# Kernel tuning notes

Hardware: AMD Instinct MI355X
Metric: run time of the kernel (lower is better)

## Reference

```python
import jax, jax.numpy as jnp
import numpy as np

B, L, N, D, H, F = 8, 12, 207, 512, 8, 2048
OUT_LEN, NG, ORDER = 12, 3, 2
EPS = 1e-6


def _ln(x, g, b):
    m = x.mean(-1, keepdims=True)
    v = x.var(-1, keepdims=True)
    return (x - m) / jnp.sqrt(v + 1e-5) * g + b


def _lin_attn(xq, xkv, w, b):
    # STLinearAttention (mask_flag=False): phi(x)=elu(x)+1 linear attention
    q = xq @ w[0] + b[0]
    k = xkv @ w[1] + b[1]
    v = xkv @ w[2] + b[2]
    Bq, Tq, Dm = q.shape
    Tk = k.shape[1]
    E = Dm // H
    q = q.reshape(Bq, Tq, H, E)
    k = k.reshape(Bq, Tk, H, E)
    v = v.reshape(Bq, Tk, H, E)
    qf = jax.nn.elu(q) + 1.0
    kf = jax.nn.elu(k) + 1.0
    kv = jnp.einsum('bshe,bshd->bhed', kf, v)
    z = 1.0 / (jnp.einsum('bthe,bhe->bth', qf, kf.sum(1)) + EPS)
    o = jnp.einsum('bthe,bhed->bthd', qf, kv) * z[..., None]
    return o.reshape(Bq, Tq, Dm) @ w[3] + b[3]


def _forward(x, st, x_mark, adj_mats, enc_qkvo_w, enc_qkvo_b, enc_ffn_w1, enc_ffn_b1,
             enc_ffn_w2, enc_ffn_b2, enc_ln_g, enc_ln_b, dec_self_w, dec_self_b,
             dec_cross_w, dec_cross_b, dec_ffn_w1, dec_ffn_b1, dec_ffn_w2, dec_ffn_b2,
             dec_ln_g, dec_ln_b, tt_w, tt_b, ts_w, ts_b, gcn_w, gcn_b, gcn_bn_g, gcn_bn_b):
    Bq, Lq, Nq, Dm = x.shape
    # ---- temporal encoder layer over flattened (L*N) tokens ----
    xt = x.reshape(Bq, Lq * Nq, Dm)
    h = xt + _lin_attn(xt, xt, enc_qkvo_w, enc_qkvo_b)
    y = _ln(h, enc_ln_g[0], enc_ln_b[0])
    f = jax.nn.gelu(y @ enc_ffn_w1 + enc_ffn_b1) @ enc_ffn_w2 + enc_ffn_b2
    t_out = _ln(y + f, enc_ln_g[1], enc_ln_b[1])
    # ---- spatial decoder layer: self-attn on st, cross-attn to t_out ----
    mem = t_out
    q = st.reshape(Bq, Lq * Nq, Dm)
    q = _ln(q + _lin_attn(q, q, dec_self_w, dec_self_b), dec_ln_g[0], dec_ln_b[0])
    q = _ln(q + _lin_attn(q, mem, dec_cross_w, dec_cross_b), dec_ln_g[1], dec_ln_b[1])
    f = jax.nn.gelu(q @ dec_ffn_w1 + dec_ffn_b1) @ dec_ffn_w2 + dec_ffn_b2
    s_out = _ln(q + f, dec_ln_g[2], dec_ln_b[2]).reshape(Bq, Lq, Nq, Dm)
    t_out = t_out.reshape(Bq, Lq, Nq, Dm)
    # ---- 1x1 conv projections: seq_len->out_len and d_model->nodes ----
    t_out2 = jnp.einsum('ol,blnd->bond', tt_w, t_out) + tt_b[None, :, None, None]  # [B,O,N,D]
    s_out2 = jnp.einsum('md,blnd->blnm', ts_w, s_out) + ts_b                       # [B,L,N,N]
    # ---- per-timestep NGraphConv with static + learned adaptive adjacency ----
    xg = jnp.swapaxes(t_out2, 2, 3)  # [B,O,D,N]
    feats = [xg]
    for s in range(NG):  # static supports, ORDER hops each
        A = adj_mats[:, :, s]
        hcur = xg
        for _ in range(ORDER):
            hcur = jnp.einsum('bodn,nm->bodm', hcur, A)
            feats.append(hcur)
    Aad = s_out2[:, :OUT_LEN]  # learned adaptive adjacency per timestep [B,O,N,N]
    hcur = xg
    for _ in range(ORDER):
        hcur = jnp.einsum('bodn,bonm->bodm', hcur, Aad)
        feats.append(hcur)
    cat = jnp.concatenate(feats, axis=2)  # [B,O,(NG+1)*ORDER*D+D, N] = [B,O,9D,N]
    g = jnp.einsum('odc,bocn->bodn', gcn_w, cat) + gcn_b[None, :, :, None]
    g = g * gcn_bn_g[None, :, :, None] + gcn_bn_b[None, :, :, None]  # BN (eval)
    dts = jnp.swapaxes(g, 2, 3)  # [B,O,N,D]
    return dts, s_out


def setup_inputs() -> dict:
    key = jax.random.key(0)
    ks = iter(jax.random.split(key, 48))
    nrm = lambda shp, s=0.02: jax.random.normal(next(ks), shp, jnp.float32) * s
    CCAT = D * (NG + 1) * ORDER + D  # 4608
    return dict(
        x=jax.random.normal(next(ks), (B, L, N, D), jnp.float32),
        st=jax.random.normal(next(ks), (B, L, N, D), jnp.float32),
        x_mark=jax.random.normal(next(ks), (B, L, 4), jnp.float32),
        adj_mats=jax.random.uniform(next(ks), (N, N, NG), jnp.float32) / N,
        enc_qkvo_w=nrm((4, D, D)), enc_qkvo_b=jnp.zeros((4, D), jnp.float32),
        enc_ffn_w1=nrm((D, F)), enc_ffn_b1=jnp.zeros((F,), jnp.float32),
        enc_ffn_w2=nrm((F, D)), enc_ffn_b2=jnp.zeros((D,), jnp.float32),
        enc_ln_g=jnp.ones((2, D), jnp.float32), enc_ln_b=jnp.zeros((2, D), jnp.float32),
        dec_self_w=nrm((4, D, D)), dec_self_b=jnp.zeros((4, D), jnp.float32),
        dec_cross_w=nrm((4, D, D)), dec_cross_b=jnp.zeros((4, D), jnp.float32),
        dec_ffn_w1=nrm((D, F)), dec_ffn_b1=jnp.zeros((F,), jnp.float32),
        dec_ffn_w2=nrm((F, D)), dec_ffn_b2=jnp.zeros((D,), jnp.float32),
        dec_ln_g=jnp.ones((3, D), jnp.float32), dec_ln_b=jnp.zeros((3, D), jnp.float32),
        tt_w=nrm((OUT_LEN, L), 0.1), tt_b=jnp.zeros((OUT_LEN,), jnp.float32),
        ts_w=nrm((N, D), 0.05), ts_b=jnp.zeros((N,), jnp.float32),
        gcn_w=nrm((OUT_LEN, D, CCAT)), gcn_b=jnp.zeros((OUT_LEN, D), jnp.float32),
        gcn_bn_g=jnp.ones((OUT_LEN, D), jnp.float32), gcn_bn_b=jnp.zeros((OUT_LEN, D), jnp.float32),
    )


def reference(x, st, x_mark, adj_mats, enc_qkvo_w, enc_qkvo_b, enc_ffn_w1, enc_ffn_b1,
              enc_ffn_w2, enc_ffn_b2, enc_ln_g, enc_ln_b, dec_self_w, dec_self_b,
              dec_cross_w, dec_cross_b, dec_ffn_w1, dec_ffn_b1, dec_ffn_w2, dec_ffn_b2,
              dec_ln_g, dec_ln_b, tt_w, tt_b, ts_w, ts_b, gcn_w, gcn_b, gcn_bn_g, gcn_bn_b):
    return _forward(x, st, x_mark, adj_mats, enc_qkvo_w, enc_qkvo_b, enc_ffn_w1, enc_ffn_b1,
                    enc_ffn_w2, enc_ffn_b2, enc_ln_g, enc_ln_b, dec_self_w, dec_self_b,
                    dec_cross_w, dec_cross_b, dec_ffn_w1, dec_ffn_b1, dec_ffn_w2, dec_ffn_b2,
                    dec_ln_g, dec_ln_b, tt_w, tt_b, ts_w, ts_b, gcn_w, gcn_b, gcn_bn_g, gcn_bn_b)
```

## Files before the change

kernel.cpp:

```cpp
#include <hip/hip_runtime.h>
#include <hip/hip_bf16.h>
#include <cstddef>

using bf16 = __hip_bfloat16;
typedef short s8v __attribute__((ext_vector_type(8)));
typedef __bf16 b8v __attribute__((ext_vector_type(8)));
typedef float f4v __attribute__((ext_vector_type(4)));

constexpr int cB = 8, cL = 12, cN = 207, cD = 512, cH = 8, cF = 2048;
constexpr int cO = 12, cNG = 3;
constexpr int cT  = cL * cN;
constexpr int cBT = cB * cT;
constexpr int cE  = cD / cH;
constexpr size_t SZ = (size_t)cBT * cD;
constexpr long DD = (long)cD * cD;

__device__ __forceinline__ float tofl(bf16 v) { return __bfloat162float(v); }
__device__ __forceinline__ bf16 f2b(float v) { return __float2bfloat16(v); }
__device__ __forceinline__ float ldin(const void* p, size_t i, int bf) {
    return bf ? __bfloat162float(((const bf16*)p)[i]) : ((const float*)p)[i];
}
__device__ __forceinline__ void stout(void* p, size_t i, float v, int bf) {
    if (bf) ((bf16*)p)[i] = f2b(v);
    else    ((float*)p)[i] = v;
}
__device__ __forceinline__ float gelu_f(float x) {
    float x3 = x * x * x;
    return 0.5f * x * (1.f + tanhf(0.7978845608028654f * (x + 0.044715f * x3)));
}
__device__ __forceinline__ void gload16(void* lds, const void* g) {
    __builtin_amdgcn_global_load_lds(
        (const __attribute__((address_space(1))) unsigned int*)g,
        (__attribute__((address_space(3))) unsigned int*)lds,
        16, 0, 0);
}

__global__ void detect_kernel(const void* __restrict__ x, int* __restrict__ flag) {
    __shared__ float red[4];
    int t = threadIdx.x;
    float m = 0.f;
    for (int i = t; i < 1024; i += 256) {
        float v = __bfloat162float(((const bf16*)x)[i]);
        if (v != v) v = 1e30f;
        m = fmaxf(m, fabsf(v));
    }
#pragma unroll
    for (int off = 32; off; off >>= 1) m = fmaxf(m, __shfl_down(m, off));
    if ((t & 63) == 0) red[t >> 6] = m;
    __syncthreads();
    if (t == 0) {
        float mm = fmaxf(fmaxf(red[0], red[1]), fmaxf(red[2], red[3]));
        flag[0] = (mm < 1e3f) ? 1 : 0;
    }
}

__global__ void cvt_copy(bf16* __restrict__ dst, const void* __restrict__ src,
                         const int* __restrict__ fl, size_t n, size_t soff) {
    int bf = *fl;
#pragma unroll
    for (int j = 0; j < 4; ++j) {
        size_t i = (size_t)blockIdx.x * 1024 + (size_t)j * 256 + threadIdx.x;
        if (i < n) dst[i] = f2b(ldin(src, soff + i, bf));
    }
}
__global__ void cvt_tr(bf16* __restrict__ dst, const void* __restrict__ src,
                       const int* __restrict__ fl, int K, int N, size_t soff) {
    int bf = *fl;
    size_t idx = (size_t)blockIdx.x * 256 + threadIdx.x;
    if (idx >= (size_t)K * N) return;
    int n = (int)(idx / K), k = (int)(idx % K);
    dst[idx] = f2b(ldin(src, soff + (size_t)k * N + n, bf));
}

__device__ __forceinline__ void xcd_swz(unsigned& bx, unsigned& by, unsigned& bz) {
    unsigned gx = gridDim.x, gy = gridDim.y;
    unsigned nwg = gx * gy * gridDim.z;
    unsigned orig = (blockIdx.z * gy + blockIdx.y) * gx + blockIdx.x;
    unsigned q = nwg >> 3, r = nwg & 7;
    unsigned xcd = orig & 7, sub = orig >> 3;
    unsigned wg = (xcd < r ? xcd * (q + 1) : r * (q + 1) + (xcd - r) * q) + sub;
    bx = wg % gx;
    unsigned t1 = wg / gx;
    by = t1 % gy;
    bz = t1 / gy;
}

template <int BIAS, int ACT, int OUT>
__global__ __launch_bounds__(256) void mgemm_f(
    const bf16* __restrict__ Ab, const bf16* __restrict__ Bb, void* __restrict__ Cb,
    const bf16* __restrict__ bias,
    int M, int N, int K, int lda, int ldb, int ldc,
    long sA, long sB, long sC, int modA, int modB, long aoff0, long boff0)
{
    unsigned bxu, byu, bzu;
    xcd_swz(bxu, byu, bzu);
    int bz = (int)bzu;
    const bf16* A = Ab + aoff0 + (size_t)(modA ? (bz % modA) : bz) * sA;
    const bf16* B = Bb + boff0 + (size_t)(modB ? (bz % modB) : bz) * sB;
    size_t coff = (size_t)bz * sC;

    int m0 = (int)byu * 128, n0 = (int)bxu * 128;
    int tid = threadIdx.x;
    int lane = tid & 63, w = tid >> 6;
    int wm = (w & 1) * 64, wn = (w >> 1) * 64;
    int l16 = lane & 15, quad = lane >> 4;

    __shared__ short As[128 * 32];
    __shared__ short Bs[128 * 32];

    int srow = tid >> 2, scol = (tid & 3) << 3;
    int ar0 = m0 + srow;      if (ar0 >= M) ar0 = M - 1;
    int ar1 = m0 + srow + 64; if (ar1 >= M) ar1 = M - 1;
    int br0 = n0 + srow;      if (br0 >= N) br0 = N - 1;
    int br1 = n0 + srow + 64; if (br1 >= N) br1 = N - 1;
    const bf16* ap0 = A + (size_t)ar0 * lda + scol;
    const bf16* ap1 = A + (size_t)ar1 * lda + scol;
    const bf16* bp0 = B + (size_t)br0 * ldb + scol;
    const bf16* bp1 = B + (size_t)br1 * ldb + scol;
    short* al0 = &As[w * 512];
    short* al1 = &As[2048 + w * 512];
    short* bl0 = &Bs[w * 512];
    short* bl1 = &Bs[2048 + w * 512];

    f4v acc[4][4] = {};

    int nk = K >> 5;
    for (int kk = 0; kk < nk; ++kk) {
        gload16(al0, ap0);
        gload16(al1, ap1);
        gload16(bl0, bp0);
        gload16(bl1, bp1);
        ap0 += 32; ap1 += 32; bp0 += 32; bp1 += 32;
        __syncthreads();
        b8v af[4], bfr[4];
#pragma unroll
        for (int mi = 0; mi < 4; ++mi)
            af[mi] = *(const b8v*)&As[(wm + mi * 16 + l16) * 32 + quad * 8];
#pragma unroll
        for (int ni = 0; ni < 4; ++ni)
            bfr[ni] = *(const b8v*)&Bs[(wn + ni * 16 + l16) * 32 + quad * 8];
#pragma unroll
        for (int mi = 0; mi < 4; ++mi)
#pragma unroll
            for (int ni = 0; ni < 4; ++ni)
                acc[mi][ni] = __builtin_amdgcn_mfma_f32_16x16x32_bf16(af[mi], bfr[ni], acc[mi][ni], 0, 0, 0);
        __syncthreads();
    }

    bf16* Co = (bf16*)Cb;
    float* Cf = (float*)Cb;
#pragma unroll
    for (int mi = 0; mi < 4; ++mi) {
#pragma unroll
        for (int ni = 0; ni < 4; ++ni) {
            int gn = n0 + wn + ni * 16 + l16;
            float bv = 0.f;
            if (BIAS == 1 && gn < N) bv = tofl(bias[gn]);
#pragma unroll
            for (int r = 0; r < 4; ++r) {
                int gm = m0 + wm + mi * 16 + quad * 4 + r;
                if (gm < M && gn < N) {
                    float v = acc[mi][ni][r] + bv;
                    if (BIAS == 2) v += tofl(bias[gm]);
                    if (ACT == 1) v = gelu_f(v);
                    if (ACT == 2) v = v > 0.f ? v + 1.f : expf(v);
                    size_t ci = coff + (size_t)gm * ldc + gn;
                    if (OUT == 0) Co[ci] = f2b(v);
                    else if (OUT == 1) Cf[ci] = v;
                    else Cf[ci] += v;
                }
            }
        }
    }
}

template <bool TRB, int BIAS, int ACT, int OUT>
__global__ __launch_bounds__(256) void mgemm(
    const bf16* __restrict__ Ab, const bf16* __restrict__ Bb, void* __restrict__ Cb,
    const bf16* __restrict__ bias,
    int M, int N, int K, int lda, int ldb, int ldc,
    long sA, long sB, long sC, int modA, int modB, long aoff0, long boff0)
{
    unsigned bxu, byu, bzu;
    xcd_swz(bxu, byu, bzu);
    int bz = (int)bzu;
    const bf16* A = Ab + aoff0 + (size_t)(modA ? (bz % modA) : bz) * sA;
    const bf16* B = Bb + boff0 + (size_t)(modB ? (bz % modB) : bz) * sB;
    size_t coff = (size_t)bz * sC;

    int m0 = (int)byu * 128, n0 = (int)bxu * 128;
    int tid = threadIdx.x;
    int lane = tid & 63, w = tid >> 6;
    int wm = (w & 1) * 64, wn = (w >> 1) * 64;
    int l16 = lane & 15, quad = lane >> 4;

    __shared__ short Asl[128 * 40];
    __shared__ short Bsl[128 * 40];

    f4v acc[4][4] = {};

    for (int k0 = 0; k0 < K; k0 += 32) {
        for (int g = tid; g < 512; g += 256) {
            int r = g >> 2, kg = (g & 3) << 3;
            int gr = m0 + r, gk = k0 + kg;
            s8v val = {0, 0, 0, 0, 0, 0, 0, 0};
            if (gr < M) {
                const short* src = (const short*)A + (size_t)gr * lda + gk;
                if (gk + 8 <= K) val = *(const s8v*)src;
                else {
#pragma unroll
                    for (int j = 0; j < 8; ++j) if (gk + j < K) val[j] = src[j];
                }
            }
            *(s8v*)&Asl[r * 40 + kg] = val;
        }
        if (TRB) {
            for (int g = tid; g < 512; g += 256) {
                int r = g >> 2, kg = (g & 3) << 3;
                int gr = n0 + r, gk = k0 + kg;
                s8v val = {0, 0, 0, 0, 0, 0, 0, 0};
                if (gr < N) {
                    const short* src = (const short*)B + (size_t)gr * ldb + gk;
                    if (gk + 8 <= K) val = *(const s8v*)src;
                    else {
#pragma unroll
                        for (int j = 0; j < 8; ++j) if (gk + j < K) val[j] = src[j];
                    }
                }
                *(s8v*)&Bsl[r * 40 + kg] = val;
            }
        } else {
            for (int g = tid; g < 512; g += 256) {
                int kr = g >> 4, ng = (g & 15) << 3;
                int gk = k0 + kr, gn = n0 + ng;
                s8v val = {0, 0, 0, 0, 0, 0, 0, 0};
                if (gk < K) {
                    const short* src = (const short*)B + (size_t)gk * ldb + gn;
                    if (gn + 8 <= N) val = *(const s8v*)src;
                    else {
#pragma unroll
                        for (int j = 0; j < 8; ++j) if (gn + j < N) val[j] = src[j];
                    }
                }
#pragma unroll
                for (int j = 0; j < 8; ++j) Bsl[(ng + j) * 40 + kr] = val[j];
            }
        }
        __syncthreads();
        b8v af[4], bfr[4];
#pragma unroll
        for (int mi = 0; mi < 4; ++mi)
            af[mi] = *(const b8v*)&Asl[(wm + mi * 16 + l16) * 40 + quad * 8];
#pragma unroll
        for (int ni = 0; ni < 4; ++ni)
            bfr[ni] = *(const b8v*)&Bsl[(wn + ni * 16 + l16) * 40 + quad * 8];
#pragma unroll
        for (int mi = 0; mi < 4; ++mi)
#pragma unroll
            for (int ni = 0; ni < 4; ++ni)
                acc[mi][ni] = __builtin_amdgcn_mfma_f32_16x16x32_bf16(af[mi], bfr[ni], acc[mi][ni], 0, 0, 0);
        __syncthreads();
    }

    bf16* Co = (bf16*)Cb;
    float* Cf = (float*)Cb;
#pragma unroll
    for (int mi = 0; mi < 4; ++mi) {
#pragma unroll
        for (int ni = 0; ni < 4; ++ni) {
            int gn = n0 + wn + ni * 16 + l16;
            float bv = 0.f;
            if (BIAS == 1 && gn < N) bv = tofl(bias[gn]);
#pragma unroll
            for (int r = 0; r < 4; ++r) {
                int gm = m0 + wm + mi * 16 + quad * 4 + r;
                if (gm < M && gn < N) {
                    float v = acc[mi][ni][r] + bv;
                    if (BIAS == 2) v += tofl(bias[gm]);
                    if (ACT == 1) v = gelu_f(v);
                    if (ACT == 2) v = v > 0.f ? v + 1.f : expf(v);
                    size_t ci = coff + (size_t)gm * ldc + gn;
                    if (OUT == 0) Co[ci] = f2b(v);
                    else if (OUT == 1) Cf[ci] = v;
                    else Cf[ci] += v;
                }
            }
        }
    }
}

__global__ __launch_bounds__(256) void kv_part(
    const bf16* __restrict__ Kf, const bf16* __restrict__ V,
    float* __restrict__ kvp, float* __restrict__ ksp)
{
    int bh = blockIdx.x, c = blockIdx.y;
    int b = bh / cH, h = bh % cH;
    int tbase = c * 621, tend = tbase + 621;
    __shared__ float ks[32][64];
    __shared__ float vs[32][64];
    int tid = threadIdx.x;
    int e = tid >> 2, dg = tid & 3;
    float acc[16] = {};
    float ksacc = 0.f;
    for (int t0 = tbase; t0 < tend; t0 += 32) {
        for (int i = tid; i < 32 * 64; i += 256) {
            int tt = i >> 6, ee = i & 63;
            int t = t0 + tt;
            float kk = 0.f, vv = 0.f;
            if (t < tend) {
                size_t off = ((size_t)(b * cT + t)) * cD + h * cE;
                kk = tofl(Kf[off + ee]);
                vv = tofl(V[off + ee]);
            }
            ks[tt][ee] = kk;
            vs[tt][ee] = vv;
        }
        __syncthreads();
        for (int tt = 0; tt < 32; ++tt) {
            float kf = ks[tt][e];
            if (dg == 0) ksacc += kf;
#pragma unroll
            for (int j = 0; j < 16; ++j) acc[j] += kf * vs[tt][dg * 16 + j];
        }
        __syncthreads();
    }
    size_t base = (((size_t)c * 64 + bh) * cE + e) * cE;
#pragma unroll
    for (int j = 0; j < 16; ++j) kvp[base + dg * 16 + j] = acc[j];
    if (dg == 0) ksp[(size_t)c * 4096 + bh * cE + e] = ksacc;
}

__global__ void kv_reduce(const float* __restrict__ kvp, const float* __restrict__ ksp,
                          float* __restrict__ kvf, float* __restrict__ ksf)
{
    size_t idx = (size_t)blockIdx.x * 256 + threadIdx.x;
    if (idx < 262144) {
        float s = kvp[idx] + kvp[262144 + idx] + kvp[2 * 262144 + idx] + kvp[3 * 262144 + idx];
        kvf[idx] = s;
    } else if (idx < 262144 + 4096) {
        size_t i = idx - 262144;
        ksf[i] = ksp[i] + ksp[4096 + i] + ksp[2 * 4096 + i] + ksp[3 * 4096 + i];
    }
}

__global__ __launch_bounds__(64) void attn_o(
    const bf16* __restrict__ Qf, const float* __restrict__ kv,
    const float* __restrict__ ksum, bf16* __restrict__ O)
{
    int g = blockIdx.x;
    int h = g % cH;
    int bt = g / cH;
    int b = bt / cT;
    int bh = b * cH + h;
    int d = threadIdx.x;
    size_t qoff = (size_t)bt * cD + h * cE;
    __shared__ float qs[64];
    float qv = tofl(Qf[qoff + d]);
    qs[d] = qv;
    float p = qv * ksum[bh * cE + d];
#pragma unroll
    for (int s = 32; s; s >>= 1) p += __shfl_down(p, s);
    float denom = __shfl(p, 0);
    __syncthreads();
    float z = 1.f / (denom + 1e-6f);
    const float* kvp = kv + (size_t)bh * cE * cE;
    float acc = 0.f;
#pragma unroll 8
    for (int e = 0; e < 64; ++e) acc += qs[e] * kvp[e * 64 + d];
    O[qoff + d] = f2b(acc * z);
}

template <int DUAL>
__global__ __launch_bounds__(256) void add_ln(
    const bf16* __restrict__ a, const bf16* __restrict__ b,
    const bf16* __restrict__ g, const bf16* __restrict__ be,
    bf16* __restrict__ out, void* __restrict__ dyn_out,
    const int* __restrict__ fl, size_t dyn_off)
{
    int row = blockIdx.x;
    size_t base = (size_t)row * cD;
    int t = threadIdx.x;
    float x0 = tofl(a[base + t]) + tofl(b[base + t]);
    float x1 = tofl(a[base + t + 256]) + tofl(b[base + t + 256]);
    float s1 = x0 + x1, s2 = x0 * x0 + x1 * x1;
#pragma unroll
    for (int off = 32; off; off >>= 1) { s1 += __shfl_down(s1, off); s2 += __shfl_down(s2, off); }
    __shared__ float r1[4], r2[4];
    int w = t >> 6;
    if ((t & 63) == 0) { r1[w] = s1; r2[w] = s2; }
    __syncthreads();
    float S1 = r1[0] + r1[1] + r1[2] + r1[3];
    float S2 = r2[0] + r2[1] + r2[2] + r2[3];
    float mean = S1 * (1.f / cD);
    float var = S2 * (1.f / cD) - mean * mean;
    float inv = rsqrtf(var + 1e-5f);
    float y0 = (x0 - mean) * inv * tofl(g[t]) + tofl(be[t]);
    float y1 = (x1 - mean) * inv * tofl(g[t + 256]) + tofl(be[t + 256]);
    out[base + t] = f2b(y0);
    out[base + t + 256] = f2b(y1);
    if (DUAL) {
        int bf = *fl;
        stout(dyn_out, dyn_off + base + t, y0, bf);
        stout(dyn_out, dyn_off + base + t + 256, y1, bf);
    }
}

__global__ void tout2_kernel(const bf16* __restrict__ tout, const bf16* __restrict__ ttw,
                             const bf16* __restrict__ ttb, bf16* __restrict__ XT)
{
    size_t idx = (size_t)blockIdx.x * 256 + threadIdx.x;
    if (idx >= SZ) return;
    int d = idx & (cD - 1);
    size_t r = idx >> 9;
    int n = (int)(r % cN);
    size_t r2 = r / cN;
    int o = (int)(r2 % cO);
    int b = (int)(r2 / cO);
    float acc = tofl(ttb[o]);
    size_t base = ((size_t)b * cT + n) * cD + d;
#pragma unroll
    for (int l = 0; l < cL; ++l)
        acc += tofl(ttw[o * cL + l]) * tofl(tout[base + (size_t)l * cN * cD]);
    XT[idx] = f2b(acc);
}

__global__ void extract_adjT(const void* __restrict__ adj, bf16* __restrict__ At3,
                             const int* __restrict__ fl)
{
    int bf = *fl;
    int idx = blockIdx.x * 256 + threadIdx.x;
    if (idx >= cNG * cN * cN) return;
    int s = idx / (cN * cN);
    int rem = idx - s * cN * cN;
    int m = rem / cN;
    int n = rem - m * cN;
    At3[((size_t)s * cN + m) * 208 + n] = f2b(ldin(adj, (size_t)(n * cN + m) * cNG + s, bf));
}

__global__ void dts_kernel(const float* __restrict__ g, const bf16* __restrict__ gb,
                           const bf16* __restrict__ bng, const bf16* __restrict__ bnb,
                           void* __restrict__ out, const int* __restrict__ fl)
{
    int bf = *fl;
    size_t idx = (size_t)blockIdx.x * 256 + threadIdx.x;
    if (idx >= SZ) return;
    int d = idx & (cD - 1);
    size_t r = idx >> 9;
    int o = (int)((r / cN) % cO);
    int od = o * cD + d;
    float v = (g[idx] + tofl(gb[od])) * tofl(bng[od]) + tofl(bnb[od]);
    stout(out, idx, v, bf);
}

static inline dim3 g2(int M, int N, int bz) { return dim3((N + 127) / 128, (M + 127) / 128, bz); }

static void run_attn(const bf16* Aq, const bf16* Akv, const bf16* wT, const bf16* bias,
                     bf16* Q, bf16* K, bf16* V, bf16* outp,
                     float* kvp, float* ksp, float* kvf, float* ksf, hipStream_t s)
{
    mgemm_f<1, 2, 0><<<g2(cBT, cD, 1), 256, 0, s>>>(Aq,  wT,          Q, bias,          cBT, cD, cD, cD, cD, cD, 0, 0, 0, 1, 1, 0, 0);
    mgemm_f<1, 2, 0><<<g2(cBT, cD, 1), 256, 0, s>>>(Akv, wT + DD,     K, bias + cD,     cBT, cD, cD, cD, cD, cD, 0, 0, 0, 1, 1, 0, 0);
    mgemm_f<1, 0, 0><<<g2(cBT, cD, 1), 256, 0, s>>>(Akv, wT + 2 * DD, V, bias + 2 * cD, cBT, cD, cD, cD, cD, cD, 0, 0, 0, 1, 1, 0, 0);
    kv_part<<<dim3(64, 4), 256, 0, s>>>(K, V, kvp, ksp);
    kv_reduce<<<1041, 256, 0, s>>>(kvp, ksp, kvf, ksf);
    attn_o<<<cBT * cH, 64, 0, s>>>(Q, kvf, ksf, Q);
    mgemm_f<1, 0, 0><<<g2(cBT, cD, 1), 256, 0, s>>>(Q, wT + 3 * DD, outp, bias + 3 * cD, cBT, cD, cD, cD, cD, cD, 0, 0, 0, 1, 1, 0, 0);
}

static void run_ffn(const bf16* inp, const bf16* w1T, const bf16* b1,
                    const bf16* w2T, const bf16* b2, bf16* mid, bf16* outp, hipStream_t s)
{
    const int MH = cBT / 2;
    for (int h = 0; h < 2; ++h) {
        const bf16* ip = inp + (size_t)h * MH * cD;
        bf16* op = outp + (size_t)h * MH * cD;
        mgemm_f<1, 1, 0><<<g2(MH, cF, 1), 256, 0, s>>>(ip, w1T, mid, b1, MH, cF, cD, cD, cD, cF, 0, 0, 0, 1, 1, 0, 0);
        mgemm_f<1, 0, 0><<<g2(MH, cD, 1), 256, 0, s>>>(mid, w2T, op, b2, MH, cD, cF, cF, cF, cD, 0, 0, 0, 1, 1, 0, 0);
    }
}

extern "C" void kernel_launch(void* const* d_in, const int* in_sizes, int n_in,
                              void* d_out, int out_size, void* d_ws, size_t ws_size,
                              hipStream_t stream)
{
    const void* x    = d_in[0];
    const void* st   = d_in[1];
    const void* adj  = d_in[3];
    const void* eqw  = d_in[4];
    const void* eqb  = d_in[5];
    const void* ew1  = d_in[6];
    const void* eb1  = d_in[7];
    const void* ew2  = d_in[8];
    const void* eb2  = d_in[9];
    const void* elng = d_in[10];
    const void* elnb = d_in[11];
    const void* dsw  = d_in[12];
    const void* dsb  = d_in[13];
    const void* dcw  = d_in[14];
    const void* dcb  = d_in[15];
    const void* dw1  = d_in[16];
    const void* db1  = d_in[17];
    const void* dw2  = d_in[18];
    const void* db2  = d_in[19];
    const void* dlng = d_in[20];
    const void* dlnb = d_in[21];
    const void* ttw  = d_in[22];
    const void* ttb  = d_in[23];
    const void* tsw  = d_in[24];
    const void* tsb  = d_in[25];
    const void* gw   = d_in[26];
    const void* gb   = d_in[27];
    const void* bng  = d_in[28];
    const void* bnb  = d_in[29];

    bf16* P = (bf16*)d_ws;
    size_t off = 0;
    auto alloc = [&](size_t n) { size_t o = off; off += (n + 127) & ~(size_t)127; return o; };

    size_t eqwT = alloc(4 * DD);
    size_t dswT = alloc(4 * DD);
    size_t dcwT = alloc(4 * DD);
    size_t ew1T = alloc((size_t)cD * cF);
    size_t ew2T = alloc((size_t)cD * cF);
    size_t dw1T = alloc((size_t)cD * cF);
    size_t dw2T = alloc((size_t)cD * cF);
    size_t gwB  = alloc((size_t)cO * cD * 4608);
    size_t tswB = alloc((size_t)cN * cD);
    size_t xb   = alloc(SZ);
    size_t stb  = alloc(SZ);
    size_t eqbB = alloc(4 * cD), eb1B = alloc(cF), eb2B = alloc(cD);
    size_t elngB = alloc(2 * cD), elnbB = alloc(2 * cD);
    size_t dsbB = alloc(4 * cD), dcbB = alloc(4 * cD);
    size_t db1B = alloc(cF), db2B = alloc(cD);
    size_t dlngB = alloc(3 * cD), dlnbB = alloc(3 * cD);
    size_t ttwB = alloc(cO * cL), ttbB = alloc(cO), tsbB = alloc(cN);
    size_t gbB = alloc(cO * cD), bngB = alloc(cO * cD), bnbB = alloc(cO * cD);
    size_t at3 = alloc((size_t)cNG * cN * 208);
    size_t slots = alloc(6 * SZ);
    bf16* S[6];
    for (int i = 0; i < 6; ++i) S[i] = P + slots + (size_t)i * SZ;

    float* F0  = (float*)(P + off);
    float* kvp = F0;
    float* ksp = kvp + 1048576;
    float* kvf = ksp + 16384;
    float* ksf = kvf + 262144;
    int* flag  = (int*)(ksf + 4096);

    detect_kernel<<<1, 256, 0, stream>>>(x, flag);

    for (int i = 0; i < 4; ++i) {
        cvt_tr<<<1024, 256, 0, stream>>>(P + eqwT + i * DD, eqw, flag, cD, cD, (size_t)i * DD);
        cvt_tr<<<1024, 256, 0, stream>>>(P + dswT + i * DD, dsw, flag, cD, cD, (size_t)i * DD);
        cvt_tr<<<1024, 256, 0, stream>>>(P + dcwT + i * DD, dcw, flag, cD, cD, (size_t)i * DD);
    }
    cvt_tr<<<4096, 256, 0, stream>>>(P + ew1T, ew1, flag, cD, cF, 0);
    cvt_tr<<<4096, 256, 0, stream>>>(P + ew2T, ew2, flag, cF, cD, 0);
    cvt_tr<<<4096, 256, 0, stream>>>(P + dw1T, dw1, flag, cD, cF, 0);
    cvt_tr<<<4096, 256, 0, stream>>>(P + dw2T, dw2, flag, cF, cD, 0);
    cvt_copy<<<27648, 256, 0, stream>>>(P + gwB, gw, flag, (size_t)cO * cD * 4608, 0);
    cvt_copy<<<104, 256, 0, stream>>>(P + tswB, tsw, flag, (size_t)cN * cD, 0);
    cvt_copy<<<(int)((SZ + 1023) / 1024), 256, 0, stream>>>(P + xb, x, flag, SZ, 0);
    cvt_copy<<<(int)((SZ + 1023) / 1024), 256, 0, stream>>>(P + stb, st, flag, SZ, 0);
    cvt_copy<<<2, 256, 0, stream>>>(P + eqbB, eqb, flag, 4 * cD, 0);
    cvt_copy<<<2, 256, 0, stream>>>(P + eb1B, eb1, flag, cF, 0);
    cvt_copy<<<1, 256, 0, stream>>>(P + eb2B, eb2, flag, cD, 0);
    cvt_copy<<<1, 256, 0, stream>>>(P + elngB, elng, flag, 2 * cD, 0);
    cvt_copy<<<1, 256, 0, stream>>>(P + elnbB, elnb, flag, 2 * cD, 0);
    cvt_copy<<<2, 256, 0, stream>>>(P + dsbB, dsb, flag, 4 * cD, 0);
    cvt_copy<<<2, 256, 0, stream>>>(P + dcbB, dcb, flag, 4 * cD, 0);
    cvt_copy<<<2, 256, 0, stream>>>(P + db1B, db1, flag, cF, 0);
    cvt_copy<<<1, 256, 0, stream>>>(P + db2B, db2, flag, cD, 0);
    cvt_copy<<<2, 256, 0, stream>>>(P + dlngB, dlng, flag, 3 * cD, 0);
    cvt_copy<<<2, 256, 0, stream>>>(P + dlnbB, dlnb, flag, 3 * cD, 0);
    cvt_copy<<<1, 256, 0, stream>>>(P + ttwB, ttw, flag, cO * cL, 0);
    cvt_copy<<<1, 256, 0, stream>>>(P + ttbB, ttb, flag, cO, 0);
    cvt_copy<<<1, 256, 0, stream>>>(P + tsbB, tsb, flag, cN, 0);
    cvt_copy<<<6, 256, 0, stream>>>(P + gbB, gb, flag, cO * cD, 0);
    cvt_copy<<<6, 256, 0, stream>>>(P + bngB, bng, flag, cO * cD, 0);
    cvt_copy<<<6, 256, 0, stream>>>(P + bnbB, bnb, flag, cO * cD, 0);

    run_attn(P + xb, P + xb, P + eqwT, P + eqbB, S[0], S[1], S[2], S[3], kvp, ksp, kvf, ksf, stream);
    add_ln<0><<<cBT, 256, 0, stream>>>(P + xb, S[3], P + elngB, P + elnbB, S[4], nullptr, flag, 0);
    run_ffn(S[4], P + ew1T, P + eb1B, P + ew2T, P + eb2B, S[0], S[2], stream);
    add_ln<0><<<cBT, 256, 0, stream>>>(S[4], S[2], P + elngB + cD, P + elnbB + cD, S[5], nullptr, flag, 0);

    run_attn(P + stb, P + stb, P + dswT, P + dsbB, S[0], S[1], S[2], S[3], kvp, ksp, kvf, ksf, stream);
    add_ln<0><<<cBT, 256, 0, stream>>>(P + stb, S[3], P + dlngB, P + dlnbB, S[4], nullptr, flag, 0);

    run_attn(S[4], S[5], P + dcwT, P + dcbB, S[0], S[1], S[2], S[3], kvp, ksp, kvf, ksf, stream);
    add_ln<0><<<cBT, 256, 0, stream>>>(S[4], S[3], P + dlngB + cD, P + dlnbB + cD, S[4], nullptr, flag, 0);

    run_ffn(S[4], P + dw1T, P + db1B, P + dw2T, P + db2B, S[0], S[2], stream);
    add_ln<1><<<cBT, 256, 0, stream>>>(S[4], S[2], P + dlngB + 2 * cD, P + dlnbB + 2 * cD, S[3], d_out, flag, SZ);

    tout2_kernel<<<(int)(SZ / 256), 256, 0, stream>>>(S[5], P + ttwB, P + ttbB, S[0]);

    mgemm_f<2, 0, 0><<<g2(cN, cN, cB * cO), 256, 0, stream>>>(
        P + tswB, S[3], S[1], P + tsbB, cN, cN, cD, cD, cD, 208,
        0, (long)cN * cD, (long)cN * 208, 1, 0, 0, 0);

    extract_adjT<<<(cNG * cN * cN + 255) / 256, 256, 0, stream>>>(adj, P + at3, flag);

    float* G = (float*)S[4];

    auto accum = [&](const bf16* Feat, int f) {
        mgemm_f<0, 0, 2><<<g2(cN, cD, cB * cO), 256, 0, stream>>>(
            Feat, P + gwB, G, nullptr, cN, cD, cD, cD, 4608, cD,
            (long)cN * cD, (long)cD * 4608, (long)cN * cD, 0, cO, 0, (long)f * cD);
    };
    auto featmul = [&](const bf16* A, long sA, int modA, long aoff0, const bf16* Fin, bf16* Fout) {
        mgemm<false, 0, 0, 0><<<g2(cN, cD, cB * cO), 256, 0, stream>>>(
            A, Fin, Fout, nullptr, cN, cD, cN, 208, cD, cD,
            sA, (long)cN * cD, (long)cN * cD, modA, 0, aoff0, 0);
    };

    mgemm_f<0, 0, 1><<<g2(cN, cD, cB * cO), 256, 0, stream>>>(
        S[0], P + gwB, G, nullptr, cN, cD, cD, cD, 4608, cD,
        (long)cN * cD, (long)cD * 4608, (long)cN * cD, 0, cO, 0, 0);
    for (int s = 0; s < cNG; ++s) {
        featmul(P + at3, 0, 1, (long)s * cN * 208, S[0], S[3]);
        accum(S[3], 2 * s + 1);
        featmul(P + at3, 0, 1, (long)s * cN * 208, S[3], S[2]);
        accum(S[2], 2 * s + 2);
    }
    featmul(S[1], (long)cN * 208, 0, 0, S[0], S[3]);
    accum(S[3], 7);
    featmul(S[1], (long)cN * 208, 0, 0, S[3], S[2]);
    accum(S[2], 8);

    dts_kernel<<<(int)((SZ + 255) / 256), 256, 0, stream>>>(G, P + gbB, P + bngB, P + bnbB, d_out, flag);
}
```

Baseline: 2.586 ms.

## Split KV accumulation into 12 chunks, tile attention output per chunk, vectorize tout2

```diff
diff --git a/kernel.cpp b/kernel.cpp
--- a/kernel.cpp
+++ b/kernel.cpp
@@ -14,9 +14,19 @@
 constexpr int cE  = cD / cH;
 constexpr size_t SZ = (size_t)cBT * cD;
 constexpr long DD = (long)cD * cD;
+constexpr int KVCH = 12;
+constexpr int CHLEN = 207;
 
 __device__ __forceinline__ float tofl(bf16 v) { return __bfloat162float(v); }
 __device__ __forceinline__ bf16 f2b(float v) { return __float2bfloat16(v); }
+__device__ __forceinline__ float b2f_raw(short s) {
+    unsigned u = ((unsigned)(unsigned short)s) << 16;
+    float f; __builtin_memcpy(&f, &u, 4); return f;
+}
+__device__ __forceinline__ short f2b_raw(float v) {
+    bf16 t = __float2bfloat16(v);
+    short s; __builtin_memcpy(&s, &t, 2); return s;
+}
 __device__ __forceinline__ float ldin(const void* p, size_t i, int bf) {
     return bf ? __bfloat162float(((const bf16*)p)[i]) : ((const float*)p)[i];
 }
@@ -294,39 +304,51 @@
     float* __restrict__ kvp, float* __restrict__ ksp)
 {
     int bh = blockIdx.x, c = blockIdx.y;
-    int b = bh / cH, h = bh % cH;
-    int tbase = c * 621, tend = tbase + 621;
+    int b = bh >> 3, h = bh & 7;
+    int tbase = c * CHLEN, tend = tbase + CHLEN;
     __shared__ float ks[32][64];
     __shared__ float vs[32][64];
     int tid = threadIdx.x;
     int e = tid >> 2, dg = tid & 3;
-    float acc[16] = {};
+    f4v a0 = {}, a1 = {}, a2 = {}, a3 = {};
     float ksacc = 0.f;
+    int srow = tid >> 3, sc = (tid & 7) << 3;
     for (int t0 = tbase; t0 < tend; t0 += 32) {
-        for (int i = tid; i < 32 * 64; i += 256) {
-            int tt = i >> 6, ee = i & 63;
-            int t = t0 + tt;
-            float kk = 0.f, vv = 0.f;
-            if (t < tend) {
-                size_t off = ((size_t)(b * cT + t)) * cD + h * cE;
-                kk = tofl(Kf[off + ee]);
-                vv = tofl(V[off + ee]);
-            }
-            ks[tt][ee] = kk;
-            vs[tt][ee] = vv;
+        int t = t0 + srow;
+        s8v kk8 = {0, 0, 0, 0, 0, 0, 0, 0};
+        s8v vv8 = {0, 0, 0, 0, 0, 0, 0, 0};
+        if (t < tend) {
+            size_t off2 = ((size_t)(b * cT + t)) * cD + h * cE + sc;
+            kk8 = *(const s8v*)((const short*)Kf + off2);
+            vv8 = *(const s8v*)((const short*)V + off2);
         }
         __syncthreads();
+        f4v kf0, kf1, vf0, vf1;
+#pragma unroll
+        for (int j = 0; j < 4; ++j) {
+            kf0[j] = b2f_raw(kk8[j]);     kf1[j] = b2f_raw(kk8[4 + j]);
+            vf0[j] = b2f_raw(vv8[j]);     vf1[j] = b2f_raw(vv8[4 + j]);
+        }
+        *(f4v*)&ks[srow][sc] = kf0;  *(f4v*)&ks[srow][sc + 4] = kf1;
+        *(f4v*)&vs[srow][sc] = vf0;  *(f4v*)&vs[srow][sc + 4] = vf1;
+        __syncthreads();
+#pragma unroll 8
         for (int tt = 0; tt < 32; ++tt) {
             float kf = ks[tt][e];
-            if (dg == 0) ksacc += kf;
-#pragma unroll
-            for (int j = 0; j < 16; ++j) acc[j] += kf * vs[tt][dg * 16 + j];
-        }
-        __syncthreads();
-    }
-    size_t base = (((size_t)c * 64 + bh) * cE + e) * cE;
-#pragma unroll
-    for (int j = 0; j < 16; ++j) kvp[base + dg * 16 + j] = acc[j];
+            ksacc += kf;
+            const float* vp2 = &vs[tt][dg * 16];
+            f4v v0 = *(const f4v*)(vp2);
+            f4v v1 = *(const f4v*)(vp2 + 4);
+            f4v v2 = *(const f4v*)(vp2 + 8);
+            f4v v3 = *(const f4v*)(vp2 + 12);
+            a0 += kf * v0;  a1 += kf * v1;  a2 += kf * v2;  a3 += kf * v3;
+        }
+    }
+    size_t base = (((size_t)c * 64 + bh) * cE + e) * cE + dg * 16;
+    *(f4v*)&kvp[base]      = a0;
+    *(f4v*)&kvp[base + 4]  = a1;
+    *(f4v*)&kvp[base + 8]  = a2;
+    *(f4v*)&kvp[base + 12] = a3;
     if (dg == 0) ksp[(size_t)c * 4096 + bh * cE + e] = ksacc;
 }
 
@@ -335,39 +357,79 @@
 {
     size_t idx = (size_t)blockIdx.x * 256 + threadIdx.x;
     if (idx < 262144) {
-        float s = kvp[idx] + kvp[262144 + idx] + kvp[2 * 262144 + idx] + kvp[3 * 262144 + idx];
+        float s = 0.f;
+#pragma unroll
+        for (int c2 = 0; c2 < KVCH; ++c2) s += kvp[(size_t)c2 * 262144 + idx];
         kvf[idx] = s;
     } else if (idx < 262144 + 4096) {
         size_t i = idx - 262144;
-        ksf[i] = ksp[i] + ksp[4096 + i] + ksp[2 * 4096 + i] + ksp[3 * 4096 + i];
-    }
-}
-
-__global__ __launch_bounds__(64) void attn_o(
+        float s = 0.f;
+#pragma unroll
+        for (int c2 = 0; c2 < KVCH; ++c2) s += ksp[(size_t)c2 * 4096 + i];
+        ksf[i] = s;
+    }
+}
+
+__global__ __launch_bounds__(256) void attn_o2(
     const bf16* __restrict__ Qf, const float* __restrict__ kv,
     const float* __restrict__ ksum, bf16* __restrict__ O)
 {
-    int g = blockIdx.x;
-    int h = g % cH;
-    int bt = g / cH;
-    int b = bt / cT;
-    int bh = b * cH + h;
-    int d = threadIdx.x;
-    size_t qoff = (size_t)bt * cD + h * cE;
-    __shared__ float qs[64];
-    float qv = tofl(Qf[qoff + d]);
-    qs[d] = qv;
-    float p = qv * ksum[bh * cE + d];
-#pragma unroll
-    for (int s = 32; s; s >>= 1) p += __shfl_down(p, s);
-    float denom = __shfl(p, 0);
+    int c = blockIdx.x, bh = blockIdx.y;
+    int b = bh >> 3, h = bh & 7;
+    __shared__ float kvs[64][64];
+    int tid = threadIdx.x;
+    const float* kvsrc = kv + (size_t)bh * 4096;
+    for (int i = tid; i < 4096; i += 256) {
+        int e2 = i >> 6, d2 = i & 63;
+        int g = e2 >> 2;
+        kvs[d2][(((g ^ (d2 & 15)) & 15) << 2) | (e2 & 3)] = kvsrc[i];
+    }
+    int l = tid & 63, w = tid >> 6;
+    float kse = ksum[bh * 64 + l];
     __syncthreads();
-    float z = 1.f / (denom + 1e-6f);
-    const float* kvp = kv + (size_t)bh * cE * cE;
-    float acc = 0.f;
-#pragma unroll 8
-    for (int e = 0; e < 64; ++e) acc += qs[e] * kvp[e * 64 + d];
-    O[qoff + d] = f2b(acc * z);
+
+    int rbeg = w * 52;
+    int rend = (w == 3) ? CHLEN : rbeg + 52;
+    const short* Qs = (const short*)Qf;
+    for (int r0 = rbeg; r0 < rend; r0 += 4) {
+        float qv[4];
+#pragma unroll
+        for (int j = 0; j < 4; ++j) {
+            int rr = r0 + j;
+            qv[j] = (rr < rend)
+                ? b2f_raw(Qs[((size_t)(b * cT + c * CHLEN + rr)) * cD + h * cE + l])
+                : 0.f;
+        }
+        float den[4];
+#pragma unroll
+        for (int j = 0; j < 4; ++j) {
+            float p = qv[j] * kse;
+#pragma unroll
+            for (int s = 32; s; s >>= 1) p += __shfl_xor(p, s);
+            den[j] = 1.f / (p + 1e-6f);
+        }
+        float oa[4] = {0.f, 0.f, 0.f, 0.f};
+#pragma unroll
+        for (int g = 0; g < 16; ++g) {
+            f4v kvv = *(const f4v*)&kvs[l][((g ^ (l & 15)) & 15) << 2];
+#pragma unroll
+            for (int j = 0; j < 4; ++j) {
+                float q0 = __shfl(qv[j], 4 * g + 0);
+                float q1 = __shfl(qv[j], 4 * g + 1);
+                float q2 = __shfl(qv[j], 4 * g + 2);
+                float q3 = __shfl(qv[j], 4 * g + 3);
+                oa[j] += q0 * kvv[0] + q1 * kvv[1] + q2 * kvv[2] + q3 * kvv[3];
+            }
+        }
+#pragma unroll
+        for (int j = 0; j < 4; ++j) {
+            int rr = r0 + j;
+            if (rr < rend) {
+                size_t ooff = ((size_t)(b * cT + c * CHLEN + rr)) * cD + h * cE + l;
+                O[ooff] = f2b(oa[j] * den[j]);
+            }
+        }
+    }
 }
 
 template <int DUAL>
@@ -408,20 +470,31 @@
 __global__ void tout2_kernel(const bf16* __restrict__ tout, const bf16* __restrict__ ttw,
                              const bf16* __restrict__ ttb, bf16* __restrict__ XT)
 {
-    size_t idx = (size_t)blockIdx.x * 256 + threadIdx.x;
-    if (idx >= SZ) return;
-    int d = idx & (cD - 1);
-    size_t r = idx >> 9;
+    size_t idx8 = ((size_t)blockIdx.x * 256 + threadIdx.x) * 8;
+    if (idx8 >= SZ) return;
+    int d = (int)(idx8 & (cD - 1));
+    size_t r = idx8 >> 9;
     int n = (int)(r % cN);
     size_t r2 = r / cN;
     int o = (int)(r2 % cO);
     int b = (int)(r2 / cO);
-    float acc = tofl(ttb[o]);
+    float tb = tofl(ttb[o]);
+    float acc[8];
+#pragma unroll
+    for (int j = 0; j < 8; ++j) acc[j] = tb;
     size_t base = ((size_t)b * cT + n) * cD + d;
-#pragma unroll
-    for (int l = 0; l < cL; ++l)
-        acc += tofl(ttw[o * cL + l]) * tofl(tout[base + (size_t)l * cN * cD]);
-    XT[idx] = f2b(acc);
+    const short* ts = (const short*)tout;
+#pragma unroll
+    for (int l = 0; l < cL; ++l) {
+        float wv = tofl(ttw[o * cL + l]);
+        s8v v = *(const s8v*)(ts + base + (size_t)l * cN * cD);
+#pragma unroll
+        for (int j = 0; j < 8; ++j) acc[j] += wv * b2f_raw(v[j]);
+    }
+    s8v ov;
+#pragma unroll
+    for (int j = 0; j < 8; ++j) ov[j] = f2b_raw(acc[j]);
+    *(s8v*)((short*)XT + idx8) = ov;
 }
 
 __global__ void extract_adjT(const void* __restrict__ adj, bf16* __restrict__ At3,
@@ -461,9 +534,9 @@
     mgemm_f<1, 2, 0><<<g2(cBT, cD, 1), 256, 0, s>>>(Aq,  wT,          Q, bias,          cBT, cD, cD, cD, cD, cD, 0, 0, 0, 1, 1, 0, 0);
     mgemm_f<1, 2, 0><<<g2(cBT, cD, 1), 256, 0, s>>>(Akv, wT + DD,     K, bias + cD,     cBT, cD, cD, cD, cD, cD, 0, 0, 0, 1, 1, 0, 0);
     mgemm_f<1, 0, 0><<<g2(cBT, cD, 1), 256, 0, s>>>(Akv, wT + 2 * DD, V, bias + 2 * cD, cBT, cD, cD, cD, cD, cD, 0, 0, 0, 1, 1, 0, 0);
-    kv_part<<<dim3(64, 4), 256, 0, s>>>(K, V, kvp, ksp);
-    kv_reduce<<<1041, 256, 0, s>>>(kvp, ksp, kvf, ksf);
-    attn_o<<<cBT * cH, 64, 0, s>>>(Q, kvf, ksf, Q);
+    kv_part<<<dim3(64, KVCH), 256, 0, s>>>(K, V, kvp, ksp);
+    kv_reduce<<<1040, 256, 0, s>>>(kvp, ksp, kvf, ksf);
+    attn_o2<<<dim3(KVCH, 64), 256, 0, s>>>(Q, kvf, ksf, Q);
     mgemm_f<1, 0, 0><<<g2(cBT, cD, 1), 256, 0, s>>>(Q, wT + 3 * DD, outp, bias + 3 * cD, cBT, cD, cD, cD, cD, cD, 0, 0, 0, 1, 1, 0, 0);
 }
 
@@ -542,8 +615,8 @@
 
     float* F0  = (float*)(P + off);
     float* kvp = F0;
-    float* ksp = kvp + 1048576;
-    float* kvf = ksp + 16384;
+    float* ksp = kvp + (size_t)KVCH * 262144;
+    float* kvf = ksp + (size_t)KVCH * 4096;
     float* ksf = kvf + 262144;
     int* flag  = (int*)(ksf + 4096);
 
@@ -594,7 +667,7 @@
     run_ffn(S[4], P + dw1T, P + db1B, P + dw2T, P + db2B, S[0], S[2], stream);
     add_ln<1><<<cBT, 256, 0, stream>>>(S[4], S[2], P + dlngB + 2 * cD, P + dlnbB + 2 * cD, S[3], d_out, flag, SZ);
 
-    tout2_kernel<<<(int)(SZ / 256), 256, 0, stream>>>(S[5], P + ttwB, P + ttbB, S[0]);
+    tout2_kernel<<<(int)(SZ / 2048), 256, 0, stream>>>(S[5], P + ttwB, P + ttbB, S[0]);
 
     mgemm_f<2, 0, 0><<<g2(cN, cN, cB * cO), 256, 0, stream>>>(
         P + tswB, S[3], S[1], P + tsbB, cN, cN, cD, cD, cD, 208,
```

After: 2.735 ms. 1.06x slower.
